# Kernel tuning notes

Measured on AMD Instinct MI355X. Metric: run time of the kernel, lower is better.

Reference implementation:

```python
import jax, jax.numpy as jnp
import numpy as np

LRELU_GAIN = np.sqrt(2.0).astype(np.float32)  # apply_activation gain for leaky_relu


def setup_inputs() -> dict:
    key = jax.random.key(0)
    ks = jax.random.split(key, 8)
    N, H, W, C_in = 8, 256, 256, 128
    num_ws, w_dim, fmaps, kernel = 16, 512, 128, 3
    return {
        "x": jax.random.normal(ks[0], (N, H, W, C_in), dtype=jnp.float32),
        "dlatents": jax.random.normal(ks[1], (N, num_ws, w_dim), dtype=jnp.float32),
        "noise": jax.random.normal(ks[2], (N, H, W, 1), dtype=jnp.float32),
        "affine_w": jax.random.normal(ks[3], (w_dim, C_in), dtype=jnp.float32),
        "affine_b": jnp.ones((C_in,), dtype=jnp.float32),  # bias_init=1
        "conv_w": jax.random.normal(ks[4], (kernel, kernel, C_in, fmaps), dtype=jnp.float32),
        "conv_b": jax.random.normal(ks[5], (fmaps,), dtype=jnp.float32),
        "noise_strength": jax.random.uniform(ks[6], (1,), dtype=jnp.float32),
        "layer_idx": 5,
    }


def reference(x, dlatents, noise, affine_w, affine_b, conv_w, conv_b, noise_strength, layer_idx):
    # --- affine (equalized-lr Linear, lr_multiplier=1): s = z @ (W/sqrt(fan_in)) + b ---
    w_dim = affine_w.shape[0]
    z = dlatents[:, layer_idx]                                   # [N, w_dim]
    s = z @ (affine_w * np.float32(1.0 / np.sqrt(w_dim))) + affine_b   # [N, C_in]

    # --- equalized-lr conv weight: w * 1/sqrt(k*k*C_in) ---
    k, _, cin, cout = conv_w.shape
    w = conv_w * np.float32(1.0 / np.sqrt(k * k * cin))          # [k,k,Cin,Cout]

    # --- demodulation coefficient d[n,o] = rsqrt(sum_{k,k,i} (w*s)^2 + eps) ---
    d = jax.lax.rsqrt(jnp.einsum('hwio,ni->no', jnp.square(w), jnp.square(s)) + 1e-8)  # [N, Cout]

    # --- non-fused modconv: modulate input, shared conv, demodulate output ---
    xm = x * s[:, None, None, :]                                 # [N,H,W,Cin]
    y = jax.lax.conv_general_dilated(
        xm, w, window_strides=(1, 1), padding='SAME',
        dimension_numbers=('NHWC', 'HWIO', 'NHWC'))              # [N,H,W,Cout]
    y = y * d[:, None, None, :]

    # --- noise injection, bias, activation (leaky_relu 0.2 with sqrt(2) gain) ---
    y = y + noise_strength[0] * noise
    y = y + conv_b
    return jax.nn.leaky_relu(y, negative_slope=0.2) * LRELU_GAIN
```

## Files before the change

### kernel.cpp

```cpp
#include <hip/hip_runtime.h>

typedef unsigned short u16;
typedef unsigned int   u32;
typedef __bf16 v8bf __attribute__((ext_vector_type(8)));
typedef float  v4f  __attribute__((ext_vector_type(4)));

#define INV_SQRT_W   0.044194173824159216f
#define INV_SQRT_KKC 0.029462782549439483f
#define LRELU_GAIN   1.4142135623730951f

__device__ __forceinline__ u16 f2bf(float f) {
    u32 u = __float_as_uint(f);
    u = (u + 0x7fffu + ((u >> 16) & 1u)) >> 16;
    return (u16)u;
}

__device__ __forceinline__ void glds16(const u16* g, u16* l) {
    __builtin_amdgcn_global_load_lds(
        (const __attribute__((address_space(1))) void*)g,
        (__attribute__((address_space(3))) void*)l, 16, 0, 0);
}

__global__ void k_s(const float* __restrict__ dlat,
                    const float* __restrict__ aw,
                    const float* __restrict__ ab,
                    const int*   __restrict__ lidx,
                    float* __restrict__ s_out)
{
    const int n   = blockIdx.x;
    const int tid = threadIdx.x;
    const int i   = tid & 127, kh = tid >> 7;
    const int li  = lidx[0];
    const float* z = dlat + (n * 16 + li) * 512 + kh * 256;
    const float* a = aw + kh * 256 * 128 + i;
    float a0 = 0.f, a1 = 0.f, a2 = 0.f, a3 = 0.f;
    for (int k = 0; k < 256; k += 4) {
        a0 += z[k + 0] * a[(k + 0) * 128];
        a1 += z[k + 1] * a[(k + 1) * 128];
        a2 += z[k + 2] * a[(k + 2) * 128];
        a3 += z[k + 3] * a[(k + 3) * 128];
    }
    __shared__ float part[256];
    part[tid] = a0 + a1 + a2 + a3;
    __syncthreads();
    if (tid < 128)
        s_out[n * 128 + i] = (part[i] + part[i + 128]) * INV_SQRT_W + ab[i];
}

__global__ void k_w2(const float* __restrict__ cw, float* __restrict__ W2)
{
    const int idx = blockIdx.x * 256 + threadIdx.x;
    float acc = 0.f;
    #pragma unroll
    for (int t = 0; t < 9; ++t) {
        float w = cw[t * 16384 + idx];
        acc += w * w;
    }
    W2[idx] = acc * (INV_SQRT_KKC * INV_SQRT_KKC);
}

__global__ void k_d(const float* __restrict__ W2,
                    const float* __restrict__ s_buf,
                    float* __restrict__ d_out)
{
    const int n = blockIdx.x;
    const int o = threadIdx.x;
    __shared__ float s2[128];
    float sv = s_buf[n * 128 + o];
    s2[o] = sv * sv;
    __syncthreads();
    float acc = 1e-8f;
    #pragma unroll 4
    for (int i = 0; i < 128; ++i)
        acc += W2[i * 128 + o] * s2[i];
    d_out[n * 128 + o] = 1.0f / sqrtf(acc);
}

__global__ void k_wmod(const float* __restrict__ cw,
                       const float* __restrict__ s_buf,
                       const float* __restrict__ d_buf,
                       u16* __restrict__ wmod)
{
    const int b   = blockIdx.x;
    const int n   = b / 36;
    const int s   = b - n * 36;
    const int p   = (s >= 18) ? 1 : 0;
    const int sp  = s - p * 18;
    const int tap = sp >> 1, q2 = sp & 1;
    const int cibase = p * 64 + q2 * 32;
    const int tid = threadIdx.x;
    __shared__ float ssh[32], dsh[128];
    if (tid < 32)  ssh[tid] = s_buf[n * 128 + cibase + tid] * INV_SQRT_KKC;
    if (tid < 128) dsh[tid] = d_buf[n * 128 + tid];
    __syncthreads();
    u16* wt = wmod + ((size_t)b << 12);
    #pragma unroll
    for (int r = 0; r < 2; ++r) {
        int t2   = r * 256 + tid;
        int g    = t2 >> 7;
        int cout = t2 & 127;
        float dv = dsh[cout];
        u32 pk[4];
        #pragma unroll
        for (int jj = 0; jj < 4; ++jj) {
            int cl = g * 8 + jj * 2;
            float v0 = cw[((tap * 128 + cibase + cl) << 7) + cout]     * ssh[cl]     * dv;
            float v1 = cw[((tap * 128 + cibase + cl + 1) << 7) + cout] * ssh[cl + 1] * dv;
            pk[jj] = (u32)f2bf(v0) | ((u32)f2bf(v1) << 16);
        }
        *(uint4*)&wt[(g << 10) + (cout << 3)] = *(uint4*)pk;
    }
}

__global__ __launch_bounds__(256, 4) void k_conv(
    const float* __restrict__ x,
    const float* __restrict__ noise,
    const float* __restrict__ conv_b,
    const float* __restrict__ nstr,
    const u16*   __restrict__ wmod,
    float* __restrict__ out)
{
    __shared__ __align__(16) u16 xs[11520];
    __shared__ __align__(16) u16 wsh[8192];

    const int bid0 = blockIdx.x;
    const int bid  = ((bid0 & 7) << 9) + (bid0 >> 3);
    const int n   = bid >> 9;
    const int hb  = (bid >> 4) & 31;
    const int wb  = bid & 15;
    const int h0  = hb << 3, w0 = wb << 4;

    const int tid  = threadIdx.x;
    const int lane = tid & 63;
    const int wid  = tid >> 6;
    const int wm   = wid >> 1;
    const int wq   = wid & 1;
    const int lr   = lane & 15;
    const int kg   = lane >> 4;

    const float* xbase = x + ((size_t)n << 16) * 128;

    u16* const a_base = &xs[kg * 1440 + wm * 576 + lr * 8];
    u16* const b_base = &wsh[kg * 1024 + (wq * 64 + lr) * 8];

    #define STAGE_X(ph)                                                              \
    for (int t = tid; t < 1440; t += 256) {                                          \
        int q = t >> 3, g = t & 7;                                                   \
        int rr = q / 18, cc = q - rr * 18;                                           \
        int gh = h0 + rr - 1, gw = w0 + cc - 1;                                      \
        float v0=0.f,v1=0.f,v2=0.f,v3=0.f,v4=0.f,v5=0.f,v6=0.f,v7=0.f;               \
        if ((unsigned)gh < 256u && (unsigned)gw < 256u) {                            \
            const float* src = xbase + (size_t)((gh << 8) + gw) * 128                \
                               + (ph) * 64 + (g << 3);                               \
            float4 fa = *(const float4*)(src);                                       \
            float4 fb = *(const float4*)(src + 4);                                   \
            v0=fa.x; v1=fa.y; v2=fa.z; v3=fa.w; v4=fb.x; v5=fb.y; v6=fb.z; v7=fb.w;  \
        }                                                                            \
        v8bf pk;                                                                     \
        pk[0]=(__bf16)v0; pk[1]=(__bf16)v1; pk[2]=(__bf16)v2; pk[3]=(__bf16)v3;      \
        pk[4]=(__bf16)v4; pk[5]=(__bf16)v5; pk[6]=(__bf16)v6; pk[7]=(__bf16)v7;      \
        *(v8bf*)&xs[g * 1440 + q * 8] = pk;                                          \
    }

    STAGE_X(0)

    const u16* wn = wmod + ((size_t)(n * 36) << 12);
    #pragma unroll
    for (int t = 0; t < 2; ++t) {
        int chunk = wid + (t << 2);
        glds16(wn + (chunk << 9) + (lane << 3), &wsh[chunk << 9]);
    }

    v4f acc[4][4];
    #pragma unroll
    for (int a = 0; a < 4; ++a)
        #pragma unroll
        for (int b2 = 0; b2 < 4; ++b2) {
            v4f zz = {0.f, 0.f, 0.f, 0.f};
            acc[a][b2] = zz;
        }

    __syncthreads();

    #pragma unroll
    for (int s = 0; s < 36; ++s) {
        const int c = s & 1;
        if (s < 35) {
            const u16* sb = wn + ((size_t)(s + 1) << 12);
            #pragma unroll
            for (int t = 0; t < 2; ++t) {
                int chunk = wid + (t << 2);
                glds16(sb + (chunk << 9) + (lane << 3), &wsh[((c ^ 1) << 12) + (chunk << 9)]);
            }
        }
        const int sp  = (s >= 18) ? (s - 18) : s;
        const int tap = sp >> 1, q2 = sp & 1;
        const int th  = tap / 3, tw = tap - th * 3;

        v8bf af[4], bf_[4];
        #pragma unroll
        for (int mi = 0; mi < 4; ++mi)
            af[mi] = *(const v8bf*)(a_base + q2 * 5760 + (mi + th) * 144 + tw * 8);
        #pragma unroll
        for (int ni = 0; ni < 4; ++ni)
            bf_[ni] = *(const v8bf*)(b_base + (c << 12) + (ni << 7));
        #pragma unroll
        for (int mi = 0; mi < 4; ++mi)
            #pragma unroll
            for (int ni = 0; ni < 4; ++ni)
                acc[mi][ni] = __builtin_amdgcn_mfma_f32_16x16x32_bf16(
                    af[mi], bf_[ni], acc[mi][ni], 0, 0, 0);

        __syncthreads();

        if (s == 17) {
            STAGE_X(1)
            __syncthreads();
        }
    }

    const float ns = nstr[0];
    #pragma unroll
    for (int mi = 0; mi < 4; ++mi) {
        const int h = h0 + wm * 4 + mi;
        #pragma unroll
        for (int j = 0; j < 4; ++j) {
            const int w  = w0 + kg * 4 + j;
            const float nz = noise[((n << 8) + h) * 256 + w] * ns;
            float* orow = out + (size_t)((((n << 8) + h) << 8) + w) * 128;
            #pragma unroll
            for (int ni = 0; ni < 4; ++ni) {
                const int cout = wq * 64 + ni * 16 + lr;
                float v = acc[mi][ni][j] + nz + conv_b[cout];
                v = (v < 0.f ? 0.2f * v : v) * LRELU_GAIN;
                orow[cout] = v;
            }
        }
    }
}

extern "C" void kernel_launch(void* const* d_in, const int* in_sizes, int n_in,
                              void* d_out, int out_size, void* d_ws, size_t ws_size,
                              hipStream_t stream) {
    const float* x     = (const float*)d_in[0];
    const float* dlat  = (const float*)d_in[1];
    const float* noise = (const float*)d_in[2];
    const float* aw    = (const float*)d_in[3];
    const float* ab    = (const float*)d_in[4];
    const float* cw    = (const float*)d_in[5];
    const float* cb    = (const float*)d_in[6];
    const float* nstr  = (const float*)d_in[7];
    const int*   lidx  = (const int*)d_in[8];
    float* out = (float*)d_out;

    float* s_buf = (float*)d_ws;
    float* d_buf = (float*)((char*)d_ws + 4096);
    float* W2    = (float*)((char*)d_ws + 8192);
    u16*   wmod  = (u16*)((char*)d_ws + 8192);

    k_w2  <<<64,  256, 0, stream>>>(cw, W2);
    k_s   <<<8,   256, 0, stream>>>(dlat, aw, ab, lidx, s_buf);
    k_d   <<<8,   128, 0, stream>>>(W2, s_buf, d_buf);
    k_wmod<<<288, 256, 0, stream>>>(cw, s_buf, d_buf, wmod);
    k_conv<<<4096,256, 0, stream>>>(x, noise, cb, nstr, wmod, out);
}
```

Measured before the change: 217.9 us.

## Double conv tile height, read weights straight into registers, reuse A-fragments across taps

The conv tile grows from 8x16 to 16x16 output pixels per block, so each warp keeps an 8x4 accumulator grid and halo re-reads drop. Weights are no longer staged in LDS with async copies. They are loaded from global/L2 into a three-deep register prefetch ring, and the wmod layout is reordered so the vertical taps run consecutively. This lets one set of 10 A-fragment rows be reused across the three th taps, cutting LDS reads and per-step barriers. The cost is much higher register pressure (launch bounds drop to 2 blocks/CU), half as many blocks, and weight loads with global latency.

```diff
diff --git a/kernel.cpp b/kernel.cpp
--- a/kernel.cpp
+++ b/kernel.cpp
@@ -13,12 +13,6 @@
     u32 u = __float_as_uint(f);
     u = (u + 0x7fffu + ((u >> 16) & 1u)) >> 16;
     return (u16)u;
-}
-
-__device__ __forceinline__ void glds16(const u16* g, u16* l) {
-    __builtin_amdgcn_global_load_lds(
-        (const __attribute__((address_space(1))) void*)g,
-        (__attribute__((address_space(3))) void*)l, 16, 0, 0);
 }
 
 __global__ void k_s(const float* __restrict__ dlat,
@@ -84,10 +78,13 @@
     const int b   = blockIdx.x;
     const int n   = b / 36;
     const int s   = b - n * 36;
-    const int p   = (s >= 18) ? 1 : 0;
-    const int sp  = s - p * 18;
-    const int tap = sp >> 1, q2 = sp & 1;
-    const int cibase = p * 64 + q2 * 32;
+    const int ph  = s / 18;
+    const int r   = s - ph * 18;
+    const int q2  = r / 9;
+    const int rr  = r - q2 * 9;
+    const int tw  = rr / 3, th = rr - tw * 3;
+    const int tap = th * 3 + tw;
+    const int cibase = ph * 64 + q2 * 32;
     const int tid = threadIdx.x;
     __shared__ float ssh[32], dsh[128];
     if (tid < 32)  ssh[tid] = s_buf[n * 128 + cibase + tid] * INV_SQRT_KKC;
@@ -95,8 +92,8 @@
     __syncthreads();
     u16* wt = wmod + ((size_t)b << 12);
     #pragma unroll
-    for (int r = 0; r < 2; ++r) {
-        int t2   = r * 256 + tid;
+    for (int rep = 0; rep < 2; ++rep) {
+        int t2   = rep * 256 + tid;
         int g    = t2 >> 7;
         int cout = t2 & 127;
         float dv = dsh[cout];
@@ -112,7 +109,33 @@
     }
 }
 
-__global__ __launch_bounds__(256, 4) void k_conv(
+template<int T>
+__device__ __forceinline__ void conv_step(const u16* __restrict__ bp,
+                                          const u16* a_base,
+                                          v8bf af[10], v8bf bfP[3][4],
+                                          v4f acc[8][4])
+{
+    constexpr int q2 = T / 9, rr = T % 9, tw = rr / 3, th = rr % 3;
+    constexpr int slot = T % 3;
+    if constexpr (th == 0) {
+        #pragma unroll
+        for (int r = 0; r < 10; ++r)
+            af[r] = *(const v8bf*)(a_base + q2 * 10400 + r * 144 + tw * 8);
+    }
+    #pragma unroll
+    for (int mi = 0; mi < 8; ++mi)
+        #pragma unroll
+        for (int ni = 0; ni < 4; ++ni)
+            acc[mi][ni] = __builtin_amdgcn_mfma_f32_16x16x32_bf16(
+                af[mi + th], bfP[slot][ni], acc[mi][ni], 0, 0, 0);
+    if constexpr (T + 3 < 18) {
+        #pragma unroll
+        for (int ni = 0; ni < 4; ++ni)
+            bfP[slot][ni] = *(const v8bf*)(bp + (T + 3) * 4096 + ni * 128);
+    }
+}
+
+__global__ __launch_bounds__(256, 2) void k_conv(
     const float* __restrict__ x,
     const float* __restrict__ noise,
     const float* __restrict__ conv_b,
@@ -120,15 +143,14 @@
     const u16*   __restrict__ wmod,
     float* __restrict__ out)
 {
-    __shared__ __align__(16) u16 xs[11520];
-    __shared__ __align__(16) u16 wsh[8192];
+    __shared__ __align__(16) u16 xs[20800];
 
     const int bid0 = blockIdx.x;
-    const int bid  = ((bid0 & 7) << 9) + (bid0 >> 3);
-    const int n   = bid >> 9;
-    const int hb  = (bid >> 4) & 31;
-    const int wb  = bid & 15;
-    const int h0  = hb << 3, w0 = wb << 4;
+    const int bid  = ((bid0 & 7) << 8) + (bid0 >> 3);
+    const int n  = bid >> 8;
+    const int hb = (bid >> 4) & 15;
+    const int wb = bid & 15;
+    const int h0 = hb << 4, w0 = wb << 4;
 
     const int tid  = threadIdx.x;
     const int lane = tid & 63;
@@ -140,14 +162,11 @@
 
     const float* xbase = x + ((size_t)n << 16) * 128;
 
-    u16* const a_base = &xs[kg * 1440 + wm * 576 + lr * 8];
-    u16* const b_base = &wsh[kg * 1024 + (wq * 64 + lr) * 8];
-
     #define STAGE_X(ph)                                                              \
-    for (int t = tid; t < 1440; t += 256) {                                          \
+    for (int t = tid; t < 2592; t += 256) {                                          \
         int q = t >> 3, g = t & 7;                                                   \
-        int rr = q / 18, cc = q - rr * 18;                                           \
-        int gh = h0 + rr - 1, gw = w0 + cc - 1;                                      \
+        int rr_ = q / 18, cc = q - rr_ * 18;                                         \
+        int gh = h0 + rr_ - 1, gw = w0 + cc - 1;                                     \
         float v0=0.f,v1=0.f,v2=0.f,v3=0.f,v4=0.f,v5=0.f,v6=0.f,v7=0.f;               \
         if ((unsigned)gh < 256u && (unsigned)gw < 256u) {                            \
             const float* src = xbase + (size_t)((gh << 8) + gw) * 128                \
@@ -159,70 +178,63 @@
         v8bf pk;                                                                     \
         pk[0]=(__bf16)v0; pk[1]=(__bf16)v1; pk[2]=(__bf16)v2; pk[3]=(__bf16)v3;      \
         pk[4]=(__bf16)v4; pk[5]=(__bf16)v5; pk[6]=(__bf16)v6; pk[7]=(__bf16)v7;      \
-        *(v8bf*)&xs[g * 1440 + q * 8] = pk;                                          \
-    }
-
-    STAGE_X(0)
-
-    const u16* wn = wmod + ((size_t)(n * 36) << 12);
-    #pragma unroll
-    for (int t = 0; t < 2; ++t) {
-        int chunk = wid + (t << 2);
-        glds16(wn + (chunk << 9) + (lane << 3), &wsh[chunk << 9]);
-    }
-
-    v4f acc[4][4];
-    #pragma unroll
-    for (int a = 0; a < 4; ++a)
+        *(v8bf*)&xs[g * 2600 + q * 8] = pk;                                          \
+    }
+
+    u16* const a_base = &xs[kg * 2600 + (wm * 144 + lr) * 8];
+    const u16* const b_base = wmod + (size_t)n * 147456 + kg * 1024 + (wq * 64 + lr) * 8;
+
+    v4f acc[8][4];
+    #pragma unroll
+    for (int a = 0; a < 8; ++a)
         #pragma unroll
         for (int b2 = 0; b2 < 4; ++b2) {
             v4f zz = {0.f, 0.f, 0.f, 0.f};
             acc[a][b2] = zz;
         }
-
-    __syncthreads();
-
-    #pragma unroll
-    for (int s = 0; s < 36; ++s) {
-        const int c = s & 1;
-        if (s < 35) {
-            const u16* sb = wn + ((size_t)(s + 1) << 12);
-            #pragma unroll
-            for (int t = 0; t < 2; ++t) {
-                int chunk = wid + (t << 2);
-                glds16(sb + (chunk << 9) + (lane << 3), &wsh[((c ^ 1) << 12) + (chunk << 9)]);
-            }
-        }
-        const int sp  = (s >= 18) ? (s - 18) : s;
-        const int tap = sp >> 1, q2 = sp & 1;
-        const int th  = tap / 3, tw = tap - th * 3;
-
-        v8bf af[4], bf_[4];
-        #pragma unroll
-        for (int mi = 0; mi < 4; ++mi)
-            af[mi] = *(const v8bf*)(a_base + q2 * 5760 + (mi + th) * 144 + tw * 8);
-        #pragma unroll
-        for (int ni = 0; ni < 4; ++ni)
-            bf_[ni] = *(const v8bf*)(b_base + (c << 12) + (ni << 7));
-        #pragma unroll
-        for (int mi = 0; mi < 4; ++mi)
+    v8bf af[10];
+    v8bf bfP[3][4];
+
+    #pragma unroll 1
+    for (int ph = 0; ph < 2; ++ph) {
+        if (ph) __syncthreads();
+        STAGE_X(ph)
+        const u16* bp = b_base + ph * 73728;
+        #pragma unroll
+        for (int t3 = 0; t3 < 3; ++t3)
             #pragma unroll
             for (int ni = 0; ni < 4; ++ni)
-                acc[mi][ni] = __builtin_amdgcn_mfma_f32_16x16x32_bf16(
-                    af[mi], bf_[ni], acc[mi][ni], 0, 0, 0);
-
+                bfP[t3][ni] = *(const v8bf*)(bp + t3 * 4096 + ni * 128);
         __syncthreads();
 
-        if (s == 17) {
-            STAGE_X(1)
-            __syncthreads();
-        }
+        conv_step< 0>(bp, a_base, af, bfP, acc);
+        conv_step< 1>(bp, a_base, af, bfP, acc);
+        conv_step< 2>(bp, a_base, af, bfP, acc);
+        conv_step< 3>(bp, a_base, af, bfP, acc);
+        conv_step< 4>(bp, a_base, af, bfP, acc);
+        conv_step< 5>(bp, a_base, af, bfP, acc);
+        conv_step< 6>(bp, a_base, af, bfP, acc);
+        conv_step< 7>(bp, a_base, af, bfP, acc);
+        conv_step< 8>(bp, a_base, af, bfP, acc);
+        conv_step< 9>(bp, a_base, af, bfP, acc);
+        conv_step<10>(bp, a_base, af, bfP, acc);
+        conv_step<11>(bp, a_base, af, bfP, acc);
+        conv_step<12>(bp, a_base, af, bfP, acc);
+        conv_step<13>(bp, a_base, af, bfP, acc);
+        conv_step<14>(bp, a_base, af, bfP, acc);
+        conv_step<15>(bp, a_base, af, bfP, acc);
+        conv_step<16>(bp, a_base, af, bfP, acc);
+        conv_step<17>(bp, a_base, af, bfP, acc);
     }
 
     const float ns = nstr[0];
-    #pragma unroll
-    for (int mi = 0; mi < 4; ++mi) {
-        const int h = h0 + wm * 4 + mi;
+    float cb4[4];
+    #pragma unroll
+    for (int ni = 0; ni < 4; ++ni)
+        cb4[ni] = conv_b[wq * 64 + ni * 16 + lr];
+    #pragma unroll
+    for (int mi = 0; mi < 8; ++mi) {
+        const int h = h0 + wm * 8 + mi;
         #pragma unroll
         for (int j = 0; j < 4; ++j) {
             const int w  = w0 + kg * 4 + j;
@@ -231,7 +243,7 @@
             #pragma unroll
             for (int ni = 0; ni < 4; ++ni) {
                 const int cout = wq * 64 + ni * 16 + lr;
-                float v = acc[mi][ni][j] + nz + conv_b[cout];
+                float v = acc[mi][ni][j] + nz + cb4[ni];
                 v = (v < 0.f ? 0.2f * v : v) * LRELU_GAIN;
                 orow[cout] = v;
             }
@@ -262,5 +274,5 @@
     k_s   <<<8,   256, 0, stream>>>(dlat, aw, ab, lidx, s_buf);
     k_d   <<<8,   128, 0, stream>>>(W2, s_buf, d_buf);
     k_wmod<<<288, 256, 0, stream>>>(cw, s_buf, d_buf, wmod);
-    k_conv<<<4096,256, 0, stream>>>(x, noise, cb, nstr, wmod, out);
-}
+    k_conv<<<2048,256, 0, stream>>>(x, noise, cb, nstr, wmod, out);
+}
```

Result: slower. 225.8 us (+3.6%).

## Reorder conv K-steps to reuse A fragments across vertical taps and pad LDS

Applied to the files above, without the earlier changes.

The conv main loop is now fully unrolled through templated steps, and the 36 weight slices are reordered so that for each channel quarter and horizontal tap the three vertical taps run back to back. Six rows of input fragments are loaded from LDS once and reused across those three taps, instead of four fresh loads every step. The weight-modulation kernel uses the same slice order, so the weights still match. The x tile LDS stride is padded (1440 to 1448) to reduce bank conflicts, and the conv bias loads are hoisted out of the epilogue loop. Holding six A fragments raises register pressure under the 4-blocks-per-SM launch bound.

```diff
diff --git a/kernel.cpp b/kernel.cpp
--- a/kernel.cpp
+++ b/kernel.cpp
@@ -84,10 +84,11 @@
     const int b   = blockIdx.x;
     const int n   = b / 36;
     const int s   = b - n * 36;
-    const int p   = (s >= 18) ? 1 : 0;
-    const int sp  = s - p * 18;
-    const int tap = sp >> 1, q2 = sp & 1;
-    const int cibase = p * 64 + q2 * 32;
+    const int q4  = s / 9;
+    const int r   = s - q4 * 9;
+    const int tw  = r / 3, th = r - tw * 3;
+    const int tap = th * 3 + tw;
+    const int cibase = q4 * 32;
     const int tid = threadIdx.x;
     __shared__ float ssh[32], dsh[128];
     if (tid < 32)  ssh[tid] = s_buf[n * 128 + cibase + tid] * INV_SQRT_KKC;
@@ -95,8 +96,8 @@
     __syncthreads();
     u16* wt = wmod + ((size_t)b << 12);
     #pragma unroll
-    for (int r = 0; r < 2; ++r) {
-        int t2   = r * 256 + tid;
+    for (int rep = 0; rep < 2; ++rep) {
+        int t2   = rep * 256 + tid;
         int g    = t2 >> 7;
         int cout = t2 & 127;
         float dv = dsh[cout];
@@ -112,6 +113,42 @@
     }
 }
 
+template<int T>
+__device__ __forceinline__ void conv_step(const u16* __restrict__ wn,
+                                          u16* __restrict__ wsh,
+                                          const u16* a_base,
+                                          const u16* b_lane,
+                                          v8bf af[6], v4f acc[4][4],
+                                          int wid, int lane)
+{
+    constexpr int q4 = T / 9, r = T % 9, tw = r / 3, th = r % 3;
+    constexpr int c  = T & 1, hq = q4 & 1;
+    if constexpr (T < 35) {
+        #pragma unroll
+        for (int t = 0; t < 2; ++t) {
+            int chunk = wid + (t << 2);
+            glds16(wn + (T + 1) * 4096 + (chunk << 9) + (lane << 3),
+                   &wsh[((c ^ 1) << 12) + (chunk << 9) + (lane << 3)]);
+        }
+    }
+    if constexpr (th == 0) {
+        #pragma unroll
+        for (int j = 0; j < 6; ++j)
+            af[j] = *(const v8bf*)(a_base + hq * 5792 + (j * 18 + tw) * 8);
+    }
+    v8bf bf[4];
+    #pragma unroll
+    for (int ni = 0; ni < 4; ++ni)
+        bf[ni] = *(const v8bf*)(b_lane + (c << 12) + (ni << 7));
+    #pragma unroll
+    for (int mi = 0; mi < 4; ++mi)
+        #pragma unroll
+        for (int ni = 0; ni < 4; ++ni)
+            acc[mi][ni] = __builtin_amdgcn_mfma_f32_16x16x32_bf16(
+                af[mi + th], bf[ni], acc[mi][ni], 0, 0, 0);
+    __syncthreads();
+}
+
 __global__ __launch_bounds__(256, 4) void k_conv(
     const float* __restrict__ x,
     const float* __restrict__ noise,
@@ -120,7 +157,7 @@
     const u16*   __restrict__ wmod,
     float* __restrict__ out)
 {
-    __shared__ __align__(16) u16 xs[11520];
+    __shared__ __align__(16) u16 xs[11584];
     __shared__ __align__(16) u16 wsh[8192];
 
     const int bid0 = blockIdx.x;
@@ -140,14 +177,11 @@
 
     const float* xbase = x + ((size_t)n << 16) * 128;
 
-    u16* const a_base = &xs[kg * 1440 + wm * 576 + lr * 8];
-    u16* const b_base = &wsh[kg * 1024 + (wq * 64 + lr) * 8];
-
     #define STAGE_X(ph)                                                              \
     for (int t = tid; t < 1440; t += 256) {                                          \
         int q = t >> 3, g = t & 7;                                                   \
-        int rr = q / 18, cc = q - rr * 18;                                           \
-        int gh = h0 + rr - 1, gw = w0 + cc - 1;                                      \
+        int rr_ = q / 18, cc = q - rr_ * 18;                                         \
+        int gh = h0 + rr_ - 1, gw = w0 + cc - 1;                                     \
         float v0=0.f,v1=0.f,v2=0.f,v3=0.f,v4=0.f,v5=0.f,v6=0.f,v7=0.f;               \
         if ((unsigned)gh < 256u && (unsigned)gw < 256u) {                            \
             const float* src = xbase + (size_t)((gh << 8) + gw) * 128                \
@@ -159,16 +193,16 @@
         v8bf pk;                                                                     \
         pk[0]=(__bf16)v0; pk[1]=(__bf16)v1; pk[2]=(__bf16)v2; pk[3]=(__bf16)v3;      \
         pk[4]=(__bf16)v4; pk[5]=(__bf16)v5; pk[6]=(__bf16)v6; pk[7]=(__bf16)v7;      \
-        *(v8bf*)&xs[g * 1440 + q * 8] = pk;                                          \
+        *(v8bf*)&xs[g * 1448 + q * 8] = pk;                                          \
     }
 
     STAGE_X(0)
 
-    const u16* wn = wmod + ((size_t)(n * 36) << 12);
+    const u16* wn = wmod + ((size_t)n * 36) * 4096;
     #pragma unroll
     for (int t = 0; t < 2; ++t) {
         int chunk = wid + (t << 2);
-        glds16(wn + (chunk << 9) + (lane << 3), &wsh[chunk << 9]);
+        glds16(wn + (chunk << 9) + (lane << 3), &wsh[(chunk << 9) + (lane << 3)]);
     }
 
     v4f acc[4][4];
@@ -180,46 +214,58 @@
             acc[a][b2] = zz;
         }
 
-    __syncthreads();
-
-    #pragma unroll
-    for (int s = 0; s < 36; ++s) {
-        const int c = s & 1;
-        if (s < 35) {
-            const u16* sb = wn + ((size_t)(s + 1) << 12);
-            #pragma unroll
-            for (int t = 0; t < 2; ++t) {
-                int chunk = wid + (t << 2);
-                glds16(sb + (chunk << 9) + (lane << 3), &wsh[((c ^ 1) << 12) + (chunk << 9)]);
-            }
-        }
-        const int sp  = (s >= 18) ? (s - 18) : s;
-        const int tap = sp >> 1, q2 = sp & 1;
-        const int th  = tap / 3, tw = tap - th * 3;
-
-        v8bf af[4], bf_[4];
-        #pragma unroll
-        for (int mi = 0; mi < 4; ++mi)
-            af[mi] = *(const v8bf*)(a_base + q2 * 5760 + (mi + th) * 144 + tw * 8);
-        #pragma unroll
-        for (int ni = 0; ni < 4; ++ni)
-            bf_[ni] = *(const v8bf*)(b_base + (c << 12) + (ni << 7));
-        #pragma unroll
-        for (int mi = 0; mi < 4; ++mi)
-            #pragma unroll
-            for (int ni = 0; ni < 4; ++ni)
-                acc[mi][ni] = __builtin_amdgcn_mfma_f32_16x16x32_bf16(
-                    af[mi], bf_[ni], acc[mi][ni], 0, 0, 0);
-
-        __syncthreads();
-
-        if (s == 17) {
-            STAGE_X(1)
-            __syncthreads();
-        }
-    }
+    const u16* const a_base = &xs[kg * 1448 + (wm * 72 + lr) * 8];
+    const u16* const b_lane = &wsh[kg * 1024 + (wq * 64 + lr) * 8];
+
+    __syncthreads();
+
+    v8bf af[6];
+    conv_step< 0>(wn, wsh, a_base, b_lane, af, acc, wid, lane);
+    conv_step< 1>(wn, wsh, a_base, b_lane, af, acc, wid, lane);
+    conv_step< 2>(wn, wsh, a_base, b_lane, af, acc, wid, lane);
+    conv_step< 3>(wn, wsh, a_base, b_lane, af, acc, wid, lane);
+    conv_step< 4>(wn, wsh, a_base, b_lane, af, acc, wid, lane);
+    conv_step< 5>(wn, wsh, a_base, b_lane, af, acc, wid, lane);
+    conv_step< 6>(wn, wsh, a_base, b_lane, af, acc, wid, lane);
+    conv_step< 7>(wn, wsh, a_base, b_lane, af, acc, wid, lane);
+    conv_step< 8>(wn, wsh, a_base, b_lane, af, acc, wid, lane);
+    conv_step< 9>(wn, wsh, a_base, b_lane, af, acc, wid, lane);
+    conv_step<10>(wn, wsh, a_base, b_lane, af, acc, wid, lane);
+    conv_step<11>(wn, wsh, a_base, b_lane, af, acc, wid, lane);
+    conv_step<12>(wn, wsh, a_base, b_lane, af, acc, wid, lane);
+    conv_step<13>(wn, wsh, a_base, b_lane, af, acc, wid, lane);
+    conv_step<14>(wn, wsh, a_base, b_lane, af, acc, wid, lane);
+    conv_step<15>(wn, wsh, a_base, b_lane, af, acc, wid, lane);
+    conv_step<16>(wn, wsh, a_base, b_lane, af, acc, wid, lane);
+    conv_step<17>(wn, wsh, a_base, b_lane, af, acc, wid, lane);
+
+    STAGE_X(1)
+    __syncthreads();
+
+    conv_step<18>(wn, wsh, a_base, b_lane, af, acc, wid, lane);
+    conv_step<19>(wn, wsh, a_base, b_lane, af, acc, wid, lane);
+    conv_step<20>(wn, wsh, a_base, b_lane, af, acc, wid, lane);
+    conv_step<21>(wn, wsh, a_base, b_lane, af, acc, wid, lane);
+    conv_step<22>(wn, wsh, a_base, b_lane, af, acc, wid, lane);
+    conv_step<23>(wn, wsh, a_base, b_lane, af, acc, wid, lane);
+    conv_step<24>(wn, wsh, a_base, b_lane, af, acc, wid, lane);
+    conv_step<25>(wn, wsh, a_base, b_lane, af, acc, wid, lane);
+    conv_step<26>(wn, wsh, a_base, b_lane, af, acc, wid, lane);
+    conv_step<27>(wn, wsh, a_base, b_lane, af, acc, wid, lane);
+    conv_step<28>(wn, wsh, a_base, b_lane, af, acc, wid, lane);
+    conv_step<29>(wn, wsh, a_base, b_lane, af, acc, wid, lane);
+    conv_step<30>(wn, wsh, a_base, b_lane, af, acc, wid, lane);
+    conv_step<31>(wn, wsh, a_base, b_lane, af, acc, wid, lane);
+    conv_step<32>(wn, wsh, a_base, b_lane, af, acc, wid, lane);
+    conv_step<33>(wn, wsh, a_base, b_lane, af, acc, wid, lane);
+    conv_step<34>(wn, wsh, a_base, b_lane, af, acc, wid, lane);
+    conv_step<35>(wn, wsh, a_base, b_lane, af, acc, wid, lane);
 
     const float ns = nstr[0];
+    float cb4[4];
+    #pragma unroll
+    for (int ni = 0; ni < 4; ++ni)
+        cb4[ni] = conv_b[wq * 64 + ni * 16 + lr];
     #pragma unroll
     for (int mi = 0; mi < 4; ++mi) {
         const int h = h0 + wm * 4 + mi;
@@ -231,7 +277,7 @@
             #pragma unroll
             for (int ni = 0; ni < 4; ++ni) {
                 const int cout = wq * 64 + ni * 16 + lr;
-                float v = acc[mi][ni][j] + nz + conv_b[cout];
+                float v = acc[mi][ni][j] + nz + cb4[ni];
                 v = (v < 0.f ? 0.2f * v : v) * LRELU_GAIN;
                 orow[cout] = v;
             }
```

After: 211.7 us. -2.9%, faster.
